# Performance work log

Measured on AMD Instinct MI355X. Metric: run time of the kernel, lower is better.

The kernel has to match this reference:

```python
import jax, jax.numpy as jnp
import numpy as np

B, N, K = 4096, 16384, 512

def setup_inputs() -> dict:
    key = jax.random.key(0)
    x = jax.random.normal(key, (B, N), dtype=jnp.float32)
    return {"x": x, "k": K}

def reference(x, k):
    # Per-row abs top-k threshold + mask multiply (k < N assumed, matching config)
    Bsz = x.shape[0]
    flat = x.reshape(Bsz, -1)
    abs_flat = jnp.abs(flat)
    topk_vals, _ = jax.lax.top_k(abs_flat, k)          # [B, k]
    thresh = topk_vals[:, -1:]                          # [B, 1] kth largest abs value
    mask = (abs_flat >= thresh).astype(flat.dtype)
    return (flat * mask).reshape(x.shape)
```

## Files before the change

### kernel.cpp

```cpp
#include <hip/hip_runtime.h>

#define NT 512
#define ROWLEN 16384
#define PT 8
#define CAP 4096

typedef unsigned int u32x4 __attribute__((ext_vector_type(4)));

__device__ inline unsigned mbcnt64(unsigned long long m) {
  unsigned lo = __builtin_amdgcn_mbcnt_lo((unsigned)m, 0u);
  return __builtin_amdgcn_mbcnt_hi((unsigned)(m >> 32), lo);
}

template<int NB>
__device__ inline void select_bin(unsigned* hist, unsigned* wtot,
                                  unsigned* sel, unsigned tid, unsigned krem) {
  constexpr int BPT = NB / NT;
  constexpr int NW = NT / 64;
  const unsigned base = tid * BPT;
  unsigned c[BPT];
  unsigned s = 0;
#pragma unroll
  for (int i = 0; i < BPT; i++) { c[i] = hist[base + i]; s += c[i]; }

  const unsigned lane = tid & 63u;
  const unsigned wid  = tid >> 6;

  unsigned suf = s;
#pragma unroll
  for (int off = 1; off < 64; off <<= 1) {
    unsigned v = __shfl_down(suf, off);
    if (lane + off < 64) suf += v;
  }
  if (lane == 0) wtot[wid] = suf;
  __syncthreads();

  unsigned above = suf - s;
  for (unsigned w = wid + 1; w < NW; w++) above += wtot[w];

#pragma unroll
  for (int i = BPT - 1; i >= 0; i--) {
    unsigned cc = c[i];
    if (above < krem && above + cc >= krem) {
      sel[0] = base + (unsigned)i;
      sel[1] = krem - above;
    }
    above += cc;
  }
  __syncthreads();
}

__global__ __launch_bounds__(NT, 5)
void topk_act_kernel(const float* __restrict__ x, float* __restrict__ out,
                     const int* __restrict__ kp) {
  __shared__ unsigned hist1[2048];
  __shared__ unsigned hist2[1024];
  __shared__ unsigned hist3[1024];
  __shared__ unsigned cand[CAP];
  __shared__ unsigned wtot[NT / 64];
  __shared__ unsigned sel[2];
  __shared__ unsigned cnt;

  const unsigned tid = threadIdx.x;
  const unsigned k = (unsigned)*kp;
  const size_t rowoff = (size_t)blockIdx.x * (size_t)ROWLEN;
  const u32x4* __restrict__ xr = reinterpret_cast<const u32x4*>(x + rowoff);
  u32x4* __restrict__ orow     = reinterpret_cast<u32x4*>(out + rowoff);

  u32x4 d[PT];
#pragma unroll
  for (int j = 0; j < PT; j++) d[j] = __builtin_nontemporal_load(&xr[tid + j * NT]);

#pragma unroll
  for (int i = 0; i < 2048 / NT; i++) hist1[tid + i * NT] = 0u;
#pragma unroll
  for (int i = 0; i < 1024 / NT; i++) hist2[tid + i * NT] = 0u;
#pragma unroll
  for (int i = 0; i < 1024 / NT; i++) hist3[tid + i * NT] = 0u;
  if (tid == 0) cnt = 0u;
  __syncthreads();

#pragma unroll
  for (int j = 0; j < PT; j++) {
    atomicAdd(&hist1[(d[j].x << 1) >> 21], 1u);
    atomicAdd(&hist1[(d[j].y << 1) >> 21], 1u);
    atomicAdd(&hist1[(d[j].z << 1) >> 21], 1u);
    atomicAdd(&hist1[(d[j].w << 1) >> 21], 1u);
  }
  __syncthreads();
  select_bin<2048>(hist1, wtot, sel, tid, k);
  const unsigned P1 = sel[0];
  const unsigned r1 = sel[1];

  {
    auto push = [&](unsigned a) {
      bool p = (a >> 21) == P1;
      unsigned long long m = __ballot(p);
      if (m) {
        unsigned nw = (unsigned)__popcll(m);
        if (p) {
          unsigned pre = mbcnt64(m);
          unsigned b = 0;
          if (pre == 0) b = atomicAdd(&cnt, nw);
          b = __builtin_amdgcn_readfirstlane(b);
          unsigned i = b + pre;
          if (i < CAP) cand[i] = a;
        }
      }
    };
#pragma unroll
    for (int j = 0; j < PT; j++) {
      push(d[j].x << 1); push(d[j].y << 1); push(d[j].z << 1); push(d[j].w << 1);
    }
  }
  __syncthreads();
  const unsigned n = cnt;

  if (n <= CAP) {
    for (unsigned i = tid; i < n; i += NT)
      atomicAdd(&hist2[(cand[i] >> 11) & 0x3FFu], 1u);
  } else {
#pragma unroll
    for (int j = 0; j < PT; j++) {
      unsigned a;
      a = d[j].x << 1; if ((a >> 21) == P1) atomicAdd(&hist2[(a >> 11) & 0x3FFu], 1u);
      a = d[j].y << 1; if ((a >> 21) == P1) atomicAdd(&hist2[(a >> 11) & 0x3FFu], 1u);
      a = d[j].z << 1; if ((a >> 21) == P1) atomicAdd(&hist2[(a >> 11) & 0x3FFu], 1u);
      a = d[j].w << 1; if ((a >> 21) == P1) atomicAdd(&hist2[(a >> 11) & 0x3FFu], 1u);
    }
  }
  __syncthreads();
  select_bin<1024>(hist2, wtot, sel, tid, r1);
  const unsigned P2 = sel[0];
  const unsigned r2 = sel[1];

  if (n <= CAP) {
    for (unsigned i = tid; i < n; i += NT) {
      unsigned a = cand[i];
      if (((a >> 11) & 0x3FFu) == P2) atomicAdd(&hist3[(a >> 1) & 0x3FFu], 1u);
    }
  } else {
    const unsigned P12 = (P1 << 10) | P2;
#pragma unroll
    for (int j = 0; j < PT; j++) {
      unsigned a;
      a = d[j].x << 1; if ((a >> 11) == P12) atomicAdd(&hist3[(a >> 1) & 0x3FFu], 1u);
      a = d[j].y << 1; if ((a >> 11) == P12) atomicAdd(&hist3[(a >> 1) & 0x3FFu], 1u);
      a = d[j].z << 1; if ((a >> 11) == P12) atomicAdd(&hist3[(a >> 1) & 0x3FFu], 1u);
      a = d[j].w << 1; if ((a >> 11) == P12) atomicAdd(&hist3[(a >> 1) & 0x3FFu], 1u);
    }
  }
  __syncthreads();
  select_bin<1024>(hist3, wtot, sel, tid, r2);
  const unsigned Va = (P1 << 21) | (P2 << 11) | (sel[0] << 1);

#pragma unroll
  for (int j = 0; j < PT; j++) {
    u32x4 o;
    o.x = ((d[j].x << 1) >= Va) ? d[j].x : 0u;
    o.y = ((d[j].y << 1) >= Va) ? d[j].y : 0u;
    o.z = ((d[j].z << 1) >= Va) ? d[j].z : 0u;
    o.w = ((d[j].w << 1) >= Va) ? d[j].w : 0u;
    __builtin_nontemporal_store(o, &orow[tid + j * NT]);
  }
}

extern "C" void kernel_launch(void* const* d_in, const int* in_sizes, int n_in,
                              void* d_out, int out_size, void* d_ws, size_t ws_size,
                              hipStream_t stream) {
  const float* x   = (const float*)d_in[0];
  const int*   kp  = (const int*)d_in[1];
  float*       out = (float*)d_out;
  const int rows = out_size / ROWLEN;
  topk_act_kernel<<<rows, NT, 0, stream>>>(x, out, kp);
}
```

Before: 449.3 us.

## Split top-k into threshold kernel and separate mask-apply kernel

Separates the per-row threshold computation from the masking: the first kernel only loads the row, builds radix histograms and writes a per-row threshold to workspace. A second, lightweight kernel with two blocks per row rereads x and writes the masked output. The input load is no longer nontemporal, so the reread may hit in cache. The aim is to decouple the sync-heavy selection from the streaming write. The cost is an extra full read of x and a second launch.

```diff
diff --git a/kernel.cpp b/kernel.cpp
--- a/kernel.cpp
+++ b/kernel.cpp
@@ -51,8 +51,8 @@
 }
 
 __global__ __launch_bounds__(NT, 5)
-void topk_act_kernel(const float* __restrict__ x, float* __restrict__ out,
-                     const int* __restrict__ kp) {
+void topk_thresh_kernel(const float* __restrict__ x, unsigned* __restrict__ thresh,
+                        const int* __restrict__ kp) {
   __shared__ unsigned hist1[2048];
   __shared__ unsigned hist2[1024];
   __shared__ unsigned hist3[1024];
@@ -65,11 +65,10 @@
   const unsigned k = (unsigned)*kp;
   const size_t rowoff = (size_t)blockIdx.x * (size_t)ROWLEN;
   const u32x4* __restrict__ xr = reinterpret_cast<const u32x4*>(x + rowoff);
-  u32x4* __restrict__ orow     = reinterpret_cast<u32x4*>(out + rowoff);
 
   u32x4 d[PT];
 #pragma unroll
-  for (int j = 0; j < PT; j++) d[j] = __builtin_nontemporal_load(&xr[tid + j * NT]);
+  for (int j = 0; j < PT; j++) d[j] = xr[tid + j * NT];
 
 #pragma unroll
   for (int i = 0; i < 2048 / NT; i++) hist1[tid + i * NT] = 0u;
@@ -152,16 +151,28 @@
   }
   __syncthreads();
   select_bin<1024>(hist3, wtot, sel, tid, r2);
-  const unsigned Va = (P1 << 21) | (P2 << 11) | (sel[0] << 1);
 
+  if (tid == 0) thresh[blockIdx.x] = (P1 << 21) | (P2 << 11) | (sel[0] << 1);
+}
+
+__global__ __launch_bounds__(NT)
+void topk_apply_kernel(const float* __restrict__ x, const unsigned* __restrict__ thresh,
+                       float* __restrict__ out) {
+  const unsigned row  = blockIdx.x >> 1;
+  const unsigned half = blockIdx.x & 1;
+  const size_t base = (size_t)row * (size_t)ROWLEN + (size_t)half * (ROWLEN / 2);
+  const unsigned Va = thresh[row];
+  const u32x4* __restrict__ xr = reinterpret_cast<const u32x4*>(x + base);
+  u32x4* __restrict__ orow     = reinterpret_cast<u32x4*>(out + base);
 #pragma unroll
-  for (int j = 0; j < PT; j++) {
+  for (int j = 0; j < 4; j++) {
+    u32x4 v = xr[threadIdx.x + j * NT];
     u32x4 o;
-    o.x = ((d[j].x << 1) >= Va) ? d[j].x : 0u;
-    o.y = ((d[j].y << 1) >= Va) ? d[j].y : 0u;
-    o.z = ((d[j].z << 1) >= Va) ? d[j].z : 0u;
-    o.w = ((d[j].w << 1) >= Va) ? d[j].w : 0u;
-    __builtin_nontemporal_store(o, &orow[tid + j * NT]);
+    o.x = ((v.x << 1) >= Va) ? v.x : 0u;
+    o.y = ((v.y << 1) >= Va) ? v.y : 0u;
+    o.z = ((v.z << 1) >= Va) ? v.z : 0u;
+    o.w = ((v.w << 1) >= Va) ? v.w : 0u;
+    __builtin_nontemporal_store(o, &orow[threadIdx.x + j * NT]);
   }
 }
 
@@ -171,6 +182,8 @@
   const float* x   = (const float*)d_in[0];
   const int*   kp  = (const int*)d_in[1];
   float*       out = (float*)d_out;
+  unsigned*    thr = (unsigned*)d_ws;
   const int rows = out_size / ROWLEN;
-  topk_act_kernel<<<rows, NT, 0, stream>>>(x, out, kp);
+  topk_thresh_kernel<<<rows, NT, 0, stream>>>(x, thr, kp);
+  topk_apply_kernel<<<rows * 2, NT, 0, stream>>>(x, thr, out);
 }
```

Result: slower. 479.0 us (+6.6%).

## Process four rows per block with double-buffered register prefetch of next row

Applied to the files above, without the earlier changes.

Each block now handles four rows, loading the next row into a second register buffer while the current row runs its radix-select passes, so global-load latency overlaps the LDS histogram work. Barriers are replaced by a lighter LDS-only wait plus s_barrier, occupancy hint is lowered from 5 to 4, and loads are no longer nontemporal. This doubles register pressure and cuts the grid to a quarter of the blocks, which may reduce latency hiding across waves.

```diff
diff --git a/kernel.cpp b/kernel.cpp
--- a/kernel.cpp
+++ b/kernel.cpp
@@ -4,8 +4,15 @@
 #define ROWLEN 16384
 #define PT 8
 #define CAP 4096
+#define RPB 4
 
 typedef unsigned int u32x4 __attribute__((ext_vector_type(4)));
+
+__device__ inline void sync_lds() {
+  asm volatile("s_waitcnt lgkmcnt(0)" ::: "memory");
+  __builtin_amdgcn_s_barrier();
+  asm volatile("" ::: "memory");
+}
 
 __device__ inline unsigned mbcnt64(unsigned long long m) {
   unsigned lo = __builtin_amdgcn_mbcnt_lo((unsigned)m, 0u);
@@ -33,7 +40,7 @@
     if (lane + off < 64) suf += v;
   }
   if (lane == 0) wtot[wid] = suf;
-  __syncthreads();
+  sync_lds();
 
   unsigned above = suf - s;
   for (unsigned w = wid + 1; w < NW; w++) above += wtot[w];
@@ -47,10 +54,10 @@
     }
     above += cc;
   }
-  __syncthreads();
+  sync_lds();
 }
 
-__global__ __launch_bounds__(NT, 5)
+__global__ __launch_bounds__(NT, 4)
 void topk_act_kernel(const float* __restrict__ x, float* __restrict__ out,
                      const int* __restrict__ kp) {
   __shared__ unsigned hist1[2048];
@@ -63,106 +70,121 @@
 
   const unsigned tid = threadIdx.x;
   const unsigned k = (unsigned)*kp;
-  const size_t rowoff = (size_t)blockIdx.x * (size_t)ROWLEN;
-  const u32x4* __restrict__ xr = reinterpret_cast<const u32x4*>(x + rowoff);
-  u32x4* __restrict__ orow     = reinterpret_cast<u32x4*>(out + rowoff);
+  const size_t row0 = (size_t)blockIdx.x * RPB;
 
-  u32x4 d[PT];
+  u32x4 dA[PT], dB[PT];
+
+  auto load_row = [&](u32x4 (&d)[PT], unsigned r) {
+    const u32x4* __restrict__ xr =
+        reinterpret_cast<const u32x4*>(x + (row0 + r) * (size_t)ROWLEN);
 #pragma unroll
-  for (int j = 0; j < PT; j++) d[j] = __builtin_nontemporal_load(&xr[tid + j * NT]);
+    for (int j = 0; j < PT; j++) d[j] = xr[tid + j * NT];
+  };
+
+  auto process = [&](u32x4 (&d)[PT], unsigned r) {
+#pragma unroll
+    for (int i = 0; i < 2048 / NT; i++) hist1[tid + i * NT] = 0u;
+#pragma unroll
+    for (int i = 0; i < 1024 / NT; i++) { hist2[tid + i * NT] = 0u; hist3[tid + i * NT] = 0u; }
+    if (tid == 0) cnt = 0u;
+    sync_lds();
 
 #pragma unroll
-  for (int i = 0; i < 2048 / NT; i++) hist1[tid + i * NT] = 0u;
+    for (int j = 0; j < PT; j++) {
+      atomicAdd(&hist1[(d[j].x << 1) >> 21], 1u);
+      atomicAdd(&hist1[(d[j].y << 1) >> 21], 1u);
+      atomicAdd(&hist1[(d[j].z << 1) >> 21], 1u);
+      atomicAdd(&hist1[(d[j].w << 1) >> 21], 1u);
+    }
+    sync_lds();
+    select_bin<2048>(hist1, wtot, sel, tid, k);
+    const unsigned P1 = sel[0];
+    const unsigned r1 = sel[1];
+
+    {
+      auto push = [&](unsigned a) {
+        bool p = (a >> 21) == P1;
+        unsigned long long m = __ballot(p);
+        if (m) {
+          unsigned nw = (unsigned)__popcll(m);
+          if (p) {
+            unsigned pre = mbcnt64(m);
+            unsigned b = 0;
+            if (pre == 0) b = atomicAdd(&cnt, nw);
+            b = __builtin_amdgcn_readfirstlane(b);
+            unsigned i = b + pre;
+            if (i < CAP) cand[i] = a;
+          }
+        }
+      };
 #pragma unroll
-  for (int i = 0; i < 1024 / NT; i++) hist2[tid + i * NT] = 0u;
+      for (int j = 0; j < PT; j++) {
+        push(d[j].x << 1); push(d[j].y << 1); push(d[j].z << 1); push(d[j].w << 1);
+      }
+    }
+    sync_lds();
+    const unsigned n = cnt;
+
+    if (n <= CAP) {
+      for (unsigned i = tid; i < n; i += NT)
+        atomicAdd(&hist2[(cand[i] >> 11) & 0x3FFu], 1u);
+    } else {
 #pragma unroll
-  for (int i = 0; i < 1024 / NT; i++) hist3[tid + i * NT] = 0u;
-  if (tid == 0) cnt = 0u;
-  __syncthreads();
+      for (int j = 0; j < PT; j++) {
+        unsigned a;
+        a = d[j].x << 1; if ((a >> 21) == P1) atomicAdd(&hist2[(a >> 11) & 0x3FFu], 1u);
+        a = d[j].y << 1; if ((a >> 21) == P1) atomicAdd(&hist2[(a >> 11) & 0x3FFu], 1u);
+        a = d[j].z << 1; if ((a >> 21) == P1) atomicAdd(&hist2[(a >> 11) & 0x3FFu], 1u);
+        a = d[j].w << 1; if ((a >> 21) == P1) atomicAdd(&hist2[(a >> 11) & 0x3FFu], 1u);
+      }
+    }
+    sync_lds();
+    select_bin<1024>(hist2, wtot, sel, tid, r1);
+    const unsigned P2 = sel[0];
+    const unsigned r2 = sel[1];
 
+    if (n <= CAP) {
+      for (unsigned i = tid; i < n; i += NT) {
+        unsigned a = cand[i];
+        if (((a >> 11) & 0x3FFu) == P2) atomicAdd(&hist3[(a >> 1) & 0x3FFu], 1u);
+      }
+    } else {
+      const unsigned P12 = (P1 << 10) | P2;
 #pragma unroll
-  for (int j = 0; j < PT; j++) {
-    atomicAdd(&hist1[(d[j].x << 1) >> 21], 1u);
-    atomicAdd(&hist1[(d[j].y << 1) >> 21], 1u);
-    atomicAdd(&hist1[(d[j].z << 1) >> 21], 1u);
-    atomicAdd(&hist1[(d[j].w << 1) >> 21], 1u);
-  }
-  __syncthreads();
-  select_bin<2048>(hist1, wtot, sel, tid, k);
-  const unsigned P1 = sel[0];
-  const unsigned r1 = sel[1];
+      for (int j = 0; j < PT; j++) {
+        unsigned a;
+        a = d[j].x << 1; if ((a >> 11) == P12) atomicAdd(&hist3[(a >> 1) & 0x3FFu], 1u);
+        a = d[j].y << 1; if ((a >> 11) == P12) atomicAdd(&hist3[(a >> 1) & 0x3FFu], 1u);
+        a = d[j].z << 1; if ((a >> 11) == P12) atomicAdd(&hist3[(a >> 1) & 0x3FFu], 1u);
+        a = d[j].w << 1; if ((a >> 11) == P12) atomicAdd(&hist3[(a >> 1) & 0x3FFu], 1u);
+      }
+    }
+    sync_lds();
+    select_bin<1024>(hist3, wtot, sel, tid, r2);
+    const unsigned Va = (P1 << 21) | (P2 << 11) | (sel[0] << 1);
 
-  {
-    auto push = [&](unsigned a) {
-      bool p = (a >> 21) == P1;
-      unsigned long long m = __ballot(p);
-      if (m) {
-        unsigned nw = (unsigned)__popcll(m);
-        if (p) {
-          unsigned pre = mbcnt64(m);
-          unsigned b = 0;
-          if (pre == 0) b = atomicAdd(&cnt, nw);
-          b = __builtin_amdgcn_readfirstlane(b);
-          unsigned i = b + pre;
-          if (i < CAP) cand[i] = a;
-        }
-      }
-    };
+    u32x4* __restrict__ orow =
+        reinterpret_cast<u32x4*>(out + (row0 + r) * (size_t)ROWLEN);
 #pragma unroll
     for (int j = 0; j < PT; j++) {
-      push(d[j].x << 1); push(d[j].y << 1); push(d[j].z << 1); push(d[j].w << 1);
+      u32x4 v = d[j];
+      u32x4 o;
+      o.x = ((v.x << 1) >= Va) ? v.x : 0u;
+      o.y = ((v.y << 1) >= Va) ? v.y : 0u;
+      o.z = ((v.z << 1) >= Va) ? v.z : 0u;
+      o.w = ((v.w << 1) >= Va) ? v.w : 0u;
+      __builtin_nontemporal_store(o, &orow[tid + j * NT]);
     }
-  }
-  __syncthreads();
-  const unsigned n = cnt;
+  };
 
-  if (n <= CAP) {
-    for (unsigned i = tid; i < n; i += NT)
-      atomicAdd(&hist2[(cand[i] >> 11) & 0x3FFu], 1u);
-  } else {
-#pragma unroll
-    for (int j = 0; j < PT; j++) {
-      unsigned a;
-      a = d[j].x << 1; if ((a >> 21) == P1) atomicAdd(&hist2[(a >> 11) & 0x3FFu], 1u);
-      a = d[j].y << 1; if ((a >> 21) == P1) atomicAdd(&hist2[(a >> 11) & 0x3FFu], 1u);
-      a = d[j].z << 1; if ((a >> 21) == P1) atomicAdd(&hist2[(a >> 11) & 0x3FFu], 1u);
-      a = d[j].w << 1; if ((a >> 21) == P1) atomicAdd(&hist2[(a >> 11) & 0x3FFu], 1u);
-    }
-  }
-  __syncthreads();
-  select_bin<1024>(hist2, wtot, sel, tid, r1);
-  const unsigned P2 = sel[0];
-  const unsigned r2 = sel[1];
-
-  if (n <= CAP) {
-    for (unsigned i = tid; i < n; i += NT) {
-      unsigned a = cand[i];
-      if (((a >> 11) & 0x3FFu) == P2) atomicAdd(&hist3[(a >> 1) & 0x3FFu], 1u);
-    }
-  } else {
-    const unsigned P12 = (P1 << 10) | P2;
-#pragma unroll
-    for (int j = 0; j < PT; j++) {
-      unsigned a;
-      a = d[j].x << 1; if ((a >> 11) == P12) atomicAdd(&hist3[(a >> 1) & 0x3FFu], 1u);
-      a = d[j].y << 1; if ((a >> 11) == P12) atomicAdd(&hist3[(a >> 1) & 0x3FFu], 1u);
-      a = d[j].z << 1; if ((a >> 11) == P12) atomicAdd(&hist3[(a >> 1) & 0x3FFu], 1u);
-      a = d[j].w << 1; if ((a >> 11) == P12) atomicAdd(&hist3[(a >> 1) & 0x3FFu], 1u);
-    }
-  }
-  __syncthreads();
-  select_bin<1024>(hist3, wtot, sel, tid, r2);
-  const unsigned Va = (P1 << 21) | (P2 << 11) | (sel[0] << 1);
-
-#pragma unroll
-  for (int j = 0; j < PT; j++) {
-    u32x4 o;
-    o.x = ((d[j].x << 1) >= Va) ? d[j].x : 0u;
-    o.y = ((d[j].y << 1) >= Va) ? d[j].y : 0u;
-    o.z = ((d[j].z << 1) >= Va) ? d[j].z : 0u;
-    o.w = ((d[j].w << 1) >= Va) ? d[j].w : 0u;
-    __builtin_nontemporal_store(o, &orow[tid + j * NT]);
-  }
+  load_row(dA, 0);
+  load_row(dB, 1);
+  process(dA, 0);
+  load_row(dA, 2);
+  process(dB, 1);
+  load_row(dB, 3);
+  process(dA, 2);
+  process(dB, 3);
 }
 
 extern "C" void kernel_launch(void* const* d_in, const int* in_sizes, int n_in,
@@ -172,5 +194,5 @@
   const int*   kp  = (const int*)d_in[1];
   float*       out = (float*)d_out;
   const int rows = out_size / ROWLEN;
-  topk_act_kernel<<<rows, NT, 0, stream>>>(x, out, kp);
+  topk_act_kernel<<<rows / RPB, NT, 0, stream>>>(x, out, kp);
 }
```

New measurement: 464.8 us. 3.5% more time.
